# Kernel optimization log

Hardware: AMD Instinct MI355X
Metric: run time of the kernel (lower is better)

The kernel has to match this reference:

```python
import jax, jax.numpy as jnp
import numpy as np

DIM = 512
H = 4
HD = DIM // H
NPL = 2  # num_proj_layers
PS = float(np.sqrt(0.1))  # prior_strength ** 0.5


def conv1d(x, w, b):
    # x: [B,C,L], w: [O,I,3], SAME padding
    y = jax.lax.conv_general_dilated(x, w, window_strides=(1,), padding=[(1, 1)],
                                     dimension_numbers=('NCH', 'OIH', 'NCH'))
    return y + b[None, :, None]


def layernorm(x, g, b):
    m = jnp.mean(x, -1, keepdims=True)
    v = jnp.var(x, -1, keepdims=True)
    return (x - m) * jax.lax.rsqrt(v + 1e-5) * g + b


def maxpool1d(x):
    # kernel 3, stride 2, pad 1 (padded with -inf, matching torch MaxPool1d)
    return jax.lax.reduce_window(x, -jnp.inf, jax.lax.max, (1, 1, 3), (1, 1, 2),
                                 ((0, 0), (0, 0), (1, 1)))


def ds_block(x, cw, cb, g, b):
    # silu(conv) -> LN over channels -> maxpool; x: [B,C,L]
    x = jax.nn.silu(conv1d(x, cw, cb))
    x = jnp.swapaxes(layernorm(jnp.swapaxes(x, 1, 2), g, b), 1, 2)
    return maxpool1d(x)


def replicate_pad_odd(x):
    # F.pad(x, (0,0,0,1), 'replicate')[:, 1::2] on [B,S,D]
    return jnp.concatenate([x, x[:, -1:]], axis=1)[:, 1::2]


def setup_inputs() -> dict:
    key = jax.random.key(0)
    ks = jax.random.split(key, 16)
    B, Sq, Skv, C = 8, 2048, 512, DIM

    def n(k, shp, s=0.02):
        return jax.random.normal(k, shp, jnp.float32) * s

    return {
        'q_x': jax.random.normal(ks[0], (B, Sq, C), jnp.float32),
        'kv_x': jax.random.normal(ks[1], (B, Skv, C), jnp.float32),
        'q_freqs_cis': jax.random.normal(ks[2], (B, Sq, HD), jnp.float32),
        'k_freqs_cis': jax.random.normal(ks[3], (B, Skv, HD), jnp.float32),
        'mask': jnp.zeros((B, 1, (Sq + 1) // 2, Skv), jnp.float32),
        'attn_prior': jax.random.uniform(ks[4], (B, Sq, Skv), jnp.float32),
        'qds_conv_w': n(ks[5], (C, C, 3), 0.05),
        'qds_conv_b': jnp.zeros((C,), jnp.float32),
        'qds_ln_g': jnp.ones((C,), jnp.float32),
        'qds_ln_b': jnp.zeros((C,), jnp.float32),
        'qp_conv_w': n(ks[6], (NPL, C, C, 3), 0.05),
        'qp_conv_b': jnp.zeros((NPL, C), jnp.float32),
        'qp_ln_g': jnp.ones((NPL, C), jnp.float32),
        'qp_ln_b': jnp.zeros((NPL, C), jnp.float32),
        'wq': n(ks[7], (C, C)),
        'wk': n(ks[8], (C, C)),
        'wv': n(ks[9], (C, C)),
        'score_w': n(ks[10], (H, H, 45, 5), 0.02),
        'score_b': jnp.zeros((H,), jnp.float32),
        'proj_w': n(ks[11], (C, C)),
        'proj_b': jnp.zeros((C,), jnp.float32),
    }


def reference(q_x, kv_x, q_freqs_cis, k_freqs_cis, mask, attn_prior,
              qds_conv_w, qds_conv_b, qds_ln_g, qds_ln_b,
              qp_conv_w, qp_conv_b, qp_ln_g, qp_ln_b,
              wq, wk, wv, score_w, score_b, proj_w, proj_b):
    B, Sq, C = q_x.shape
    Skv = kv_x.shape[1]
    scale = HD ** -0.5

    # QueryDownsample: length Sq -> (Sq+1)//2
    x = ds_block(jnp.swapaxes(q_x, 1, 2), qds_conv_w, qds_conv_b, qds_ln_g, qds_ln_b)

    # QueryProj (note: original loop `for i in range(1, num_layers)` never uses xs[num_layers])
    xs = [x]
    for i in range(NPL):
        x = ds_block(x, qp_conv_w[i], qp_conv_b[i], qp_ln_g[i], qp_ln_b[i])
        xs.append(x)
    out = xs[0]
    for i in range(1, NPL):
        xi = jnp.repeat(xs[i], 2 ** i, axis=-1)  # nearest upsample
        out = out + xi[..., :out.shape[-1]]
    qx = jnp.swapaxes(out, 1, 2)  # [B, Sq2, C]
    Sq2 = (Sq + 1) // 2

    q = (qx @ wq.T).reshape(B, Sq2, H, HD)
    k = (kv_x @ wk.T).reshape(B, Skv, H, HD)
    v = (kv_x @ wv.T).reshape(B, Skv, H, HD)

    qf = replicate_pad_odd(q_freqs_cis)  # [B, Sq2, HD]
    q = q + qf[:, :, None] * PS
    k = k + k_freqs_cis[:, :, None] * PS

    q = jnp.swapaxes(q, 1, 2)  # [B,H,Sq2,HD]
    k = jnp.swapaxes(k, 1, 2)
    v = jnp.swapaxes(v, 1, 2)

    # gaussian attention: negative clamped squared L2 distance
    qs = q * scale
    kk = k * scale
    x2 = jnp.sum(qs * qs, -1)  # [B,H,Sq2]
    y2 = jnp.sum(kk * kk, -1)  # [B,H,Skv]
    xy = jnp.einsum('bhid,bhjd->bhij', qs, kk)
    attn = -jnp.clip(x2[..., :, None] + y2[..., None, :] - 2.0 * xy, 0.0, None)

    temp = jnp.linspace(1.0, 10.0, H).astype(attn.dtype)
    attn = attn / temp[None, :, None, None]

    # Conv2d(H,H,(45,5),padding=(22,2)) over the score map (mixes heads)
    sc = jax.lax.conv_general_dilated(attn, score_w, (1, 1), ((22, 22), (2, 2)),
                                      dimension_numbers=('NCHW', 'OIHW', 'NCHW'))
    attn = attn + sc + score_b[None, :, None, None]
    attn = attn + mask
    attn = jax.nn.softmax(attn, axis=-1)

    # prior log-fusion + renormalize
    prior = replicate_pad_odd(attn_prior)  # [B,Sq2,Skv]
    attn = jnp.exp(jnp.log(jnp.clip(attn, 1e-8, None)) +
                   jnp.log(jnp.clip(prior[:, None], 1e-8, None)))
    attn = attn / (jnp.sum(attn, -1, keepdims=True) + 1e-8)

    # nearest interpolate (Sq2 -> 2*Sq2) then crop to Sq
    attn = jnp.repeat(attn, 2, axis=2)[:, :, :Sq]  # [B,H,Sq,Skv]

    xout = jnp.einsum('bhqk,bhkd->bhqd', attn, v)
    xout = jnp.swapaxes(xout, 1, 2).reshape(B, Sq, C)
    xout = xout @ proj_w.T + proj_b
    return xout, attn
```

## Files before the change

kernel.cpp:

```cpp
#include <hip/hip_runtime.h>
#include <math.h>

#define PS_CONST 0.31622776601683794f

typedef __attribute__((ext_vector_type(8))) short short8;
typedef __attribute__((ext_vector_type(4))) float f32x4;

__device__ inline unsigned short f2b(float f) {
    unsigned u = __builtin_bit_cast(unsigned, f);
    unsigned r = (u + 0x7fffu + ((u >> 16) & 1u)) >> 16;
    return (unsigned short)r;
}
__device__ inline float b2f(unsigned short b) {
    return __builtin_bit_cast(float, (unsigned)b << 16);
}

__global__ __launch_bounds__(256) void cvt_bf16_k(const float* __restrict__ in,
                                                  ushort* __restrict__ out, int n4)
{
    int idx = blockIdx.x * 256 + threadIdx.x;
    if (idx >= n4) return;
    float4 vv = ((const float4*)in)[idx];
    ushort4 o;
    o.x = f2b(vv.x); o.y = f2b(vv.y); o.z = f2b(vv.z); o.w = f2b(vv.w);
    ((ushort4*)out)[idx] = o;
}

__global__ __launch_bounds__(256) void split_bf16_k(const float* __restrict__ in,
    ushort* __restrict__ hi, ushort* __restrict__ lo, int n4)
{
    int idx = blockIdx.x * 256 + threadIdx.x;
    if (idx >= n4) return;
    float4 vv = ((const float4*)in)[idx];
    float vs[4] = {vv.x, vv.y, vv.z, vv.w};
    ushort4 h, l;
    unsigned short hb; float hf;
    hb = f2b(vs[0]); hf = b2f(hb); h.x = hb; l.x = f2b(vs[0] - hf);
    hb = f2b(vs[1]); hf = b2f(hb); h.y = hb; l.y = f2b(vs[1] - hf);
    hb = f2b(vs[2]); hf = b2f(hb); h.z = hb; l.z = f2b(vs[2] - hf);
    hb = f2b(vs[3]); hf = b2f(hb); h.w = hb; l.w = f2b(vs[3] - hf);
    ((ushort4*)hi)[idx] = h;
    ((ushort4*)lo)[idx] = l;
}

__global__ __launch_bounds__(256) void wcvt_k(const float* __restrict__ w,
                                              ushort* __restrict__ out)
{
    int idx = blockIdx.x * 256 + threadIdx.x;
    if (idx >= 786432) return;
    int c = idx / 1536;
    int rem = idx - c * 1536;
    int tap = rem >> 9, i = rem & 511;
    out[idx] = f2b(w[c * 1536 + i * 3 + tap]);
}

__global__ __launch_bounds__(256) void wcvt4_k(
    const float* __restrict__ w0, const float* __restrict__ w1,
    const float* __restrict__ w2, const float* __restrict__ w3,
    ushort* __restrict__ o0, ushort* __restrict__ o1,
    ushort* __restrict__ o2, ushort* __restrict__ o3)
{
    int idx = blockIdx.x * 256 + threadIdx.x;
    int sel = idx >> 16, off = idx & 65535;
    const float* w = (sel == 0) ? w0 : (sel == 1) ? w1 : (sel == 2) ? w2 : w3;
    ushort* o = (sel == 0) ? o0 : (sel == 1) ? o1 : (sel == 2) ? o2 : o3;
    float4 vv = ((const float4*)w)[off];
    ushort4 r;
    r.x = f2b(vv.x); r.y = f2b(vv.y); r.z = f2b(vv.z); r.w = f2b(vv.w);
    ((ushort4*)o)[off] = r;
}

__global__ __launch_bounds__(256) void atoep_k(const float* __restrict__ sw,
                                               ushort* __restrict__ At)
{
    int idx = blockIdx.x * 256 + threadIdx.x;
    if (idx >= 81920) return;
    int t = idx & 7;
    int lane = (idx >> 3) & 63;
    int ks = (idx >> 9) & 1;
    int rem = idx >> 10;
    int dj = rem % 5, ohi = rem / 5;
    int m = lane & 15;
    int k = ks * 32 + ((lane >> 4) << 3) + t;
    int d = k - m;
    float val = (d >= 0 && d < 45) ? sw[(ohi * 45 + d) * 5 + dj] : 0.f;
    At[idx] = f2b(val);
}

__global__ __launch_bounds__(256) void conv_mfma(
    const ushort* __restrict__ xtb, const ushort* __restrict__ wtb,
    const float* __restrict__ cb, float* __restrict__ z, int L)
{
    __shared__ __align__(16) ushort Ash[128 * 40];
    __shared__ __align__(16) ushort Bsh[128 * 40];
    const int b = blockIdx.z;
    const int cm = blockIdx.y << 7;
    const int l0 = blockIdx.x << 7;
    const int tid = threadIdx.x;
    const int wave = tid >> 6, lane = tid & 63;
    const int wm = (wave & 1) << 6, wn = (wave >> 1) << 6;
    const int lo16 = lane & 15, hi4 = lane >> 4;

    f32x4 acc[4][4];
    #pragma unroll
    for (int i = 0; i < 4; i++)
        #pragma unroll
        for (int j = 0; j < 4; j++)
            acc[i][j] = (f32x4){0.f, 0.f, 0.f, 0.f};

    for (int k0 = 0; k0 < 1536; k0 += 32) {
        const int tap = k0 >> 9;
        const int cbase = k0 & 511;
        {
            int u = tid;
            #pragma unroll
            for (int p = 0; p < 2; p++, u += 256) {
                int row = u >> 2, g = (u & 3) << 3;
                *(uint4*)&Ash[row * 40 + g] =
                    *(const uint4*)&wtb[(size_t)(cm + row) * 1536 + k0 + g];
            }
        }
        {
            int u = tid;
            #pragma unroll
            for (int p = 0; p < 2; p++, u += 256) {
                int row = u >> 2, g = (u & 3) << 3;
                int lg = l0 + tap - 1 + row;
                uint4 val = make_uint4(0u, 0u, 0u, 0u);
                if (lg >= 0 && lg < L)
                    val = *(const uint4*)&xtb[((size_t)b * L + lg) * 512 + cbase + g];
                *(uint4*)&Bsh[row * 40 + g] = val;
            }
        }
        __syncthreads();
        short8 a[4], bb[4];
        #pragma unroll
        for (int t = 0; t < 4; t++) {
            a[t]  = *(const short8*)&Ash[(wm + t * 16 + lo16) * 40 + hi4 * 8];
            bb[t] = *(const short8*)&Bsh[(wn + t * 16 + lo16) * 40 + hi4 * 8];
        }
        #pragma unroll
        for (int mt = 0; mt < 4; mt++)
            #pragma unroll
            for (int nt = 0; nt < 4; nt++)
                acc[mt][nt] = __builtin_amdgcn_mfma_f32_16x16x32_bf16(
                    a[mt], bb[nt], acc[mt][nt], 0, 0, 0);
        __syncthreads();
    }
    #pragma unroll
    for (int mt = 0; mt < 4; mt++) {
        #pragma unroll
        for (int r = 0; r < 4; r++) {
            int c = cm + wm + mt * 16 + hi4 * 4 + r;
            float bias = cb[c];
            #pragma unroll
            for (int nt = 0; nt < 4; nt++) {
                int l = l0 + wn + nt * 16 + lo16;
                float u = acc[mt][nt][r] + bias;
                u = u / (1.f + __expf(-u));
                z[((size_t)b * 512 + c) * L + l] = u;
            }
        }
    }
}

__global__ __launch_bounds__(256) void gemm_mfma_bf16(
    const ushort* __restrict__ Xb, const ushort* __restrict__ Wb,
    const float* __restrict__ bias, float* __restrict__ Y,
    int M, int N, int K, int dup)
{
    __shared__ __align__(16) ushort Ash[128 * 40];
    __shared__ __align__(16) ushort Bsh[128 * 40];
    const int bm = blockIdx.y << 7, bn = blockIdx.x << 7;
    const int tid = threadIdx.x;
    const int wave = tid >> 6, lane = tid & 63;
    const int wm = (wave & 1) << 6, wn = (wave >> 1) << 6;
    const int lo16 = lane & 15, hi4 = lane >> 4;

    f32x4 acc[4][4];
    #pragma unroll
    for (int i = 0; i < 4; i++)
        #pragma unroll
        for (int j = 0; j < 4; j++)
            acc[i][j] = (f32x4){0.f, 0.f, 0.f, 0.f};

    for (int k0 = 0; k0 < K; k0 += 32) {
        int u = tid;
        #pragma unroll
        for (int p = 0; p < 2; p++, u += 256) {
            int row = u >> 2, g = (u & 3) << 3;
            *(uint4*)&Ash[row * 40 + g] =
                *(const uint4*)&Xb[(size_t)(bm + row) * K + k0 + g];
            *(uint4*)&Bsh[row * 40 + g] =
                *(const uint4*)&Wb[(size_t)(bn + row) * K + k0 + g];
        }
        __syncthreads();
        short8 a[4], bb[4];
        #pragma unroll
        for (int t = 0; t < 4; t++) {
            a[t]  = *(const short8*)&Ash[(wm + t * 16 + lo16) * 40 + hi4 * 8];
            bb[t] = *(const short8*)&Bsh[(wn + t * 16 + lo16) * 40 + hi4 * 8];
        }
        #pragma unroll
        for (int mt = 0; mt < 4; mt++)
            #pragma unroll
            for (int nt = 0; nt < 4; nt++)
                acc[mt][nt] = __builtin_amdgcn_mfma_f32_16x16x32_bf16(
                    a[mt], bb[nt], acc[mt][nt], 0, 0, 0);
        __syncthreads();
    }
    #pragma unroll
    for (int mt = 0; mt < 4; mt++) {
        #pragma unroll
        for (int r = 0; r < 4; r++) {
            int m = bm + wm + mt * 16 + hi4 * 4 + r;
            #pragma unroll
            for (int nt = 0; nt < 4; nt++) {
                int n = bn + wn + nt * 16 + lo16;
                float val = acc[mt][nt][r];
                if (bias) val += bias[n];
                if (dup) {
                    Y[(size_t)(2 * m)     * N + n] = val;
                    Y[(size_t)(2 * m + 1) * N + n] = val;
                } else {
                    Y[(size_t)m * N + n] = val;
                }
            }
        }
    }
}

__global__ __launch_bounds__(256) void ln_stats_k(const float* __restrict__ z,
                                                  float2* __restrict__ stats, int L)
{
    __shared__ float s_sh[4][64];
    __shared__ float s2_sh[4][64];
    const int b = blockIdx.y;
    const int colL = threadIdx.x & 63;
    const int col = (blockIdx.x << 6) + colL;
    const int part = threadIdx.x >> 6;
    const float* base = z + ((size_t)b * 512 + part * 128) * L + col;
    float s = 0.f, s2 = 0.f;
    for (int i = 0; i < 128; i++) {
        float vv = base[(size_t)i * L];
        s += vv; s2 += vv * vv;
    }
    s_sh[part][colL] = s; s2_sh[part][colL] = s2;
    __syncthreads();
    if (threadIdx.x < 64) {
        float ts = 0.f, ts2 = 0.f;
        #pragma unroll
        for (int p = 0; p < 4; p++) { ts += s_sh[p][colL]; ts2 += s2_sh[p][colL]; }
        float m = ts * (1.f / 512.f);
        float var = ts2 * (1.f / 512.f) - m * m;
        stats[(size_t)b * L + col] = make_float2(m, rsqrtf(var + 1e-5f));
    }
}

__global__ __launch_bounds__(256) void ln_maxpool_k(
    const float* __restrict__ z, const float2* __restrict__ stats,
    const float* __restrict__ g, const float* __restrict__ be,
    float* __restrict__ out, int L, int lshift)
{
    const int Lout = 1 << lshift;
    size_t idx = (size_t)blockIdx.x * 256 + threadIdx.x;
    int lp = (int)(idx & (Lout - 1));
    int c = (int)((idx >> lshift) & 511);
    int b = (int)(idx >> (lshift + 9));
    const float* zp = z + ((size_t)b * 512 + c) * L;
    const float2* sp = stats + (size_t)b * L;
    float gc = g[c], bc = be[c];
    int l = lp << 1;
    float2 st = sp[l];
    float m = (zp[l] - st.x) * st.y * gc + bc;
    if (l > 0) {
        float2 s0 = sp[l - 1];
        m = fmaxf(m, (zp[l - 1] - s0.x) * s0.y * gc + bc);
    }
    float2 s1 = sp[l + 1];
    m = fmaxf(m, (zp[l + 1] - s1.x) * s1.y * gc + bc);
    out[idx] = m;
}

__global__ __launch_bounds__(256) void transpose_cvt_k(const float* __restrict__ x0,
                                                       ushort* __restrict__ xtb)
{
    __shared__ ushort t[32][33];
    const int b = blockIdx.z, c0 = blockIdx.y << 5, l0 = blockIdx.x << 5;
    const int col = threadIdx.x & 31, r0 = threadIdx.x >> 5;
    #pragma unroll
    for (int p = 0; p < 4; p++) {
        int r = r0 + p * 8;
        t[r][col] = f2b(x0[((size_t)b * 512 + c0 + r) * 1024 + l0 + col]);
    }
    __syncthreads();
    #pragma unroll
    for (int p = 0; p < 4; p++) {
        int r = r0 + p * 8;
        xtb[((size_t)b * 1024 + l0 + r) * 512 + c0 + col] = t[col][r];
    }
}

__global__ __launch_bounds__(256) void vT_cvt_k(const float* __restrict__ v,
                                                ushort* __restrict__ vTb)
{
    __shared__ ushort t[32][33];
    const int bh = blockIdx.z, b = bh >> 2, h = bh & 3;
    const int d0 = blockIdx.y << 5, j0 = blockIdx.x << 5;
    const int col = threadIdx.x & 31, r0 = threadIdx.x >> 5;
    #pragma unroll
    for (int p = 0; p < 4; p++) {
        int r = r0 + p * 8;
        t[r][col] = f2b(v[(((size_t)b * 512 + j0 + r) * 4 + h) * 128 + d0 + col]);
    }
    __syncthreads();
    #pragma unroll
    for (int p = 0; p < 4; p++) {
        int r = r0 + p * 8;
        vTb[((size_t)bh * 128 + d0 + r) * 512 + j0 + col] = t[col][r];
    }
}

__global__ __launch_bounds__(256) void upsample_add_t(const float* __restrict__ x0,
    const float* __restrict__ x1, ushort* __restrict__ qxb)
{
    size_t idx = (size_t)blockIdx.x * 256 + threadIdx.x;
    int c = (int)(idx & 511);
    int l = (int)((idx >> 9) & 1023);
    int b = (int)(idx >> 19);
    qxb[idx] = f2b(x0[((size_t)b * 512 + c) * 1024 + l] +
                   x1[((size_t)b * 512 + c) * 512 + (l >> 1)]);
}

__global__ __launch_bounds__(256) void add_freq_q_k(float* __restrict__ q, const float* __restrict__ qf)
{
    size_t idx = (size_t)blockIdx.x * 256 + threadIdx.x;
    int d = (int)(idx & 127);
    int l = (int)((idx >> 9) & 1023);
    int b = (int)(idx >> 19);
    q[idx] += PS_CONST * qf[((size_t)b * 2048 + 2 * l + 1) * 128 + d];
}

__global__ __launch_bounds__(256) void add_freq_k_k(float* __restrict__ k, const float* __restrict__ kf)
{
    size_t idx = (size_t)blockIdx.x * 256 + threadIdx.x;
    int d = (int)(idx & 127);
    int j = (int)((idx >> 9) & 511);
    int b = (int)(idx >> 18);
    k[idx] += PS_CONST * kf[((size_t)b * 512 + j) * 128 + d];
}

__global__ __launch_bounds__(64) void rownorm_k(const float* __restrict__ X,
                                                float* __restrict__ out, int Li)
{
    int i = blockIdx.x, bh = blockIdx.y;
    int b = bh >> 2, h = bh & 3;
    const float* row = X + (((size_t)b * Li + i) * 4 + h) * 128;
    int lane = threadIdx.x;
    float v0 = row[lane], v1 = row[lane + 64];
    float s = v0 * v0 + v1 * v1;
    #pragma unroll
    for (int off = 32; off > 0; off >>= 1) s += __shfl_down(s, off);
    if (lane == 0) out[(size_t)bh * Li + i] = s;
}

__global__ __launch_bounds__(256) void scores_mfma(
    const ushort* __restrict__ qhi, const ushort* __restrict__ qlo,
    const ushort* __restrict__ khi, const ushort* __restrict__ klo,
    const float* __restrict__ q2, const float* __restrict__ k2,
    float* __restrict__ attn0)
{
    __shared__ __align__(16) ushort Ah[128 * 40];
    __shared__ __align__(16) ushort Al[128 * 40];
    __shared__ __align__(16) ushort Bh[128 * 40];
    __shared__ __align__(16) ushort Bl[128 * 40];
    const int bh = blockIdx.z, b = bh >> 2, h = bh & 3;
    const int bm = blockIdx.y << 7, bn = blockIdx.x << 7;
    const int tid = threadIdx.x;
    const int wave = tid >> 6, lane = tid & 63;
    const int wm = (wave & 1) << 6, wn = (wave >> 1) << 6;
    const int lo16 = lane & 15, hi4 = lane >> 4;

    f32x4 acc[4][4];
    #pragma unroll
    for (int i = 0; i < 4; i++)
        #pragma unroll
        for (int j = 0; j < 4; j++)
            acc[i][j] = (f32x4){0.f, 0.f, 0.f, 0.f};

    for (int k0 = 0; k0 < 128; k0 += 32) {
        int u = tid;
        #pragma unroll
        for (int p = 0; p < 2; p++, u += 256) {
            int row = u >> 2, g = (u & 3) << 3;
            size_t aoff = (((size_t)b * 1024 + bm + row) * 4 + h) * 128 + k0 + g;
            size_t boff = (((size_t)b * 512  + bn + row) * 4 + h) * 128 + k0 + g;
            *(uint4*)&Ah[row * 40 + g] = *(const uint4*)&qhi[aoff];
            *(uint4*)&Al[row * 40 + g] = *(const uint4*)&qlo[aoff];
            *(uint4*)&Bh[row * 40 + g] = *(const uint4*)&khi[boff];
            *(uint4*)&Bl[row * 40 + g] = *(const uint4*)&klo[boff];
        }
        __syncthreads();
        short8 ah[4], al[4], bhF[4], blF[4];
        #pragma unroll
        for (int t = 0; t < 4; t++) {
            int ar = (wm + t * 16 + lo16) * 40 + hi4 * 8;
            int br = (wn + t * 16 + lo16) * 40 + hi4 * 8;
            ah[t]  = *(const short8*)&Ah[ar];
            al[t]  = *(const short8*)&Al[ar];
            bhF[t] = *(const short8*)&Bh[br];
            blF[t] = *(const short8*)&Bl[br];
        }
        #pragma unroll
        for (int mt = 0; mt < 4; mt++)
            #pragma unroll
            for (int nt = 0; nt < 4; nt++) {
                acc[mt][nt] = __builtin_amdgcn_mfma_f32_16x16x32_bf16(
                    ah[mt], bhF[nt], acc[mt][nt], 0, 0, 0);
                acc[mt][nt] = __builtin_amdgcn_mfma_f32_16x16x32_bf16(
                    ah[mt], blF[nt], acc[mt][nt], 0, 0, 0);
                acc[mt][nt] = __builtin_amdgcn_mfma_f32_16x16x32_bf16(
                    al[mt], bhF[nt], acc[mt][nt], 0, 0, 0);
            }
        __syncthreads();
    }
    const float it = (h == 0) ? 1.f : (h == 1) ? 0.25f : (h == 2) ? (1.f / 7.f) : 0.1f;
    #pragma unroll
    for (int mt = 0; mt < 4; mt++) {
        #pragma unroll
        for (int r = 0; r < 4; r++) {
            int i = bm + wm + mt * 16 + hi4 * 4 + r;
            float q2v = q2[(size_t)bh * 1024 + i];
            #pragma unroll
            for (int nt = 0; nt < 4; nt++) {
                int j = bn + wn + nt * 16 + lo16;
                float d2 = q2v + k2[(size_t)bh * 512 + j] - 2.f * acc[mt][nt][r];
                d2 *= (1.f / 128.f);
                if (d2 < 0.f) d2 = 0.f;
                attn0[((size_t)bh * 1024 + i) * 512 + j] = -d2 * it;
            }
        }
    }
}

__global__ __launch_bounds__(256) void score_conv_mfma(
    const float* __restrict__ attn0, const ushort* __restrict__ At,
    const float* __restrict__ sb, const float* __restrict__ mask,
    float* __restrict__ attn1)
{
    __shared__ __align__(16) ushort tileT[4 * 36 * 120];
    const int b = blockIdx.z, i0 = blockIdx.y << 6, j0 = blockIdx.x << 5;
    const int tid = threadIdx.x, wave = tid >> 6, lane = tid & 63;

    for (int idx = tid; idx < 4 * 36 * 56; idx += 256) {
        int jj = idx % 36;
        int r2 = idx / 36;
        int ip = r2 % 56, hi = r2 / 56;
        int ii = ip << 1;
        int gi = i0 - 22 + ii, gj = j0 - 2 + jj;
        const float* src = attn0 + ((size_t)(b * 4 + hi) * 1024 + gi) * 512 + gj;
        bool jv = (unsigned)gj < 512u;
        float v0 = (jv && (unsigned)gi       < 1024u) ? src[0]   : 0.f;
        float v1 = (jv && (unsigned)(gi + 1) < 1024u) ? src[512] : 0.f;
        unsigned pk = (unsigned)f2b(v0) | ((unsigned)f2b(v1) << 16);
        *(unsigned*)&tileT[(hi * 36 + jj) * 120 + ii] = pk;
    }
    __syncthreads();

    const int n16 = lane & 15, quad = lane >> 4;
    f32x4 acc[4][2];
    #pragma unroll
    for (int o = 0; o < 4; o++)
        #pragma unroll
        for (int t = 0; t < 2; t++)
            acc[o][t] = (f32x4){0.f, 0.f, 0.f, 0.f};

    const int iibase = wave * 16 + quad * 8;
    #pragma unroll 1
    for (int hi = 0; hi < 4; hi++) {
        #pragma unroll 1
        for (int dj = 0; dj < 5; dj++) {
            #pragma unroll
            for (int ks = 0; ks < 2; ks++) {
                short8 bf[2];
                #pragma unroll
                for (int t = 0; t < 2; t++)
                    bf[t] = *(const short8*)&tileT[(hi * 36 + t * 16 + n16 + dj) * 120
                                                   + iibase + ks * 32];
                #pragma unroll
                for (int o = 0; o < 4; o++) {
                    short8 af = *(const short8*)&At[((((o * 4 + hi) * 5 + dj) * 2 + ks) * 64
                                                     + lane) * 8];
                    #pragma unroll
                    for (int t = 0; t < 2; t++)
                        acc[o][t] = __builtin_amdgcn_mfma_f32_16x16x32_bf16(
                            af, bf[t], acc[o][t], 0, 0, 0);
                }
            }
        }
    }

    #pragma unroll
    for (int o = 0; o < 4; o++) {
        float bo = sb[o];
        #pragma unroll
        for (int r = 0; r < 4; r++) {
            int i = i0 + wave * 16 + quad * 4 + r;
            size_t obase = ((size_t)(b * 4 + o) * 1024 + i) * 512;
            size_t mbase = ((size_t)b * 1024 + i) * 512;
            #pragma unroll
            for (int t = 0; t < 2; t++) {
                int j = j0 + t * 16 + n16;
                attn1[obase + j] = attn0[obase + j] + acc[o][t][r] + bo + mask[mbase + j];
            }
        }
    }
}

__global__ __launch_bounds__(256) void softmax_prior_k(
    const float* __restrict__ attn1, const float* __restrict__ prior,
    float* __restrict__ attn_out, ushort* __restrict__ ab)
{
    const int wid = threadIdx.x >> 6, lane = threadIdx.x & 63;
    size_t row = (size_t)blockIdx.x * 4 + wid;
    int i = (int)(row & 1023);
    int bh = (int)(row >> 10);
    int b = bh >> 2;
    const float* arow = attn1 + row * 512;
    const float* prow = prior + ((size_t)b * 2048 + 2 * i + 1) * 512;
    float v[8], p[8];
    #pragma unroll
    for (int t = 0; t < 8; t++) {
        v[t] = arow[lane + 64 * t];
        p[t] = prow[lane + 64 * t];
    }
    float mx = v[0];
    #pragma unroll
    for (int t = 1; t < 8; t++) mx = fmaxf(mx, v[t]);
    #pragma unroll
    for (int off = 32; off > 0; off >>= 1) mx = fmaxf(mx, __shfl_xor(mx, off));
    float sum = 0.f;
    #pragma unroll
    for (int t = 0; t < 8; t++) { v[t] = expf(v[t] - mx); sum += v[t]; }
    #pragma unroll
    for (int off = 32; off > 0; off >>= 1) sum += __shfl_xor(sum, off);
    float inv = 1.f / sum;
    float sum2 = 0.f;
    #pragma unroll
    for (int t = 0; t < 8; t++) {
        float sm = fmaxf(v[t] * inv, 1e-8f);
        float pr = fmaxf(p[t], 1e-8f);
        v[t] = sm * pr;
        sum2 += v[t];
    }
    #pragma unroll
    for (int off = 32; off > 0; off >>= 1) sum2 += __shfl_xor(sum2, off);
    float inv2 = 1.f / (sum2 + 1e-8f);
    float* o0 = attn_out + ((size_t)bh * 2048 + 2 * i) * 512;
    ushort* abrow = ab + row * 512;
    #pragma unroll
    for (int t = 0; t < 8; t++) {
        float val = v[t] * inv2;
        o0[lane + 64 * t] = val;
        o0[512 + lane + 64 * t] = val;
        abrow[lane + 64 * t] = f2b(val);
    }
}

__global__ __launch_bounds__(256) void attnv_mfma(
    const ushort* __restrict__ ab, const ushort* __restrict__ vTb,
    ushort* __restrict__ xpb)
{
    __shared__ __align__(16) ushort Ash[128 * 40];
    __shared__ __align__(16) ushort Bsh[128 * 40];
    const int bh = blockIdx.z, b = bh >> 2, h = bh & 3;
    const int bm = blockIdx.y << 7;
    const ushort* A = ab + (size_t)bh * 1024 * 512;
    const ushort* B = vTb + (size_t)bh * 128 * 512;
    const int tid = threadIdx.x;
    const int wave = tid >> 6, lane = tid & 63;
    const int wm = (wave & 1) << 6, wn = (wave >> 1) << 6;
    const int lo16 = lane & 15, hi4 = lane >> 4;

    f32x4 acc[4][4];
    #pragma unroll
    for (int i = 0; i < 4; i++)
        #pragma unroll
        for (int j = 0; j < 4; j++)
            acc[i][j] = (f32x4){0.f, 0.f, 0.f, 0.f};

    for (int k0 = 0; k0 < 512; k0 += 32) {
        int u = tid;
        #pragma unroll
        for (int p = 0; p < 2; p++, u += 256) {
            int row = u >> 2, g = (u & 3) << 3;
            *(uint4*)&Ash[row * 40 + g] = *(const uint4*)&A[(size_t)(bm + row) * 512 + k0 + g];
            *(uint4*)&Bsh[row * 40 + g] = *(const uint4*)&B[(size_t)row * 512 + k0 + g];
        }
        __syncthreads();
        short8 a[4], bb[4];
        #pragma unroll
        for (int t = 0; t < 4; t++) {
            a[t]  = *(const short8*)&Ash[(wm + t * 16 + lo16) * 40 + hi4 * 8];
            bb[t] = *(const short8*)&Bsh[(wn + t * 16 + lo16) * 40 + hi4 * 8];
        }
        #pragma unroll
        for (int mt = 0; mt < 4; mt++)
            #pragma unroll
            for (int nt = 0; nt < 4; nt++)
                acc[mt][nt] = __builtin_amdgcn_mfma_f32_16x16x32_bf16(
                    a[mt], bb[nt], acc[mt][nt], 0, 0, 0);
        __syncthreads();
    }
    #pragma unroll
    for (int mt = 0; mt < 4; mt++) {
        #pragma unroll
        for (int r = 0; r < 4; r++) {
            int m = bm + wm + mt * 16 + hi4 * 4 + r;
            #pragma unroll
            for (int nt = 0; nt < 4; nt++) {
                int n = wn + nt * 16 + lo16;
                xpb[((size_t)b * 1024 + m) * 512 + h * 128 + n] = f2b(acc[mt][nt][r]);
            }
        }
    }
}

extern "C" void kernel_launch(void* const* d_in, const int* in_sizes, int n_in,
                              void* d_out, int out_size, void* d_ws, size_t ws_size,
                              hipStream_t stream)
{
    const float* q_x    = (const float*)d_in[0];
    const float* kv_x   = (const float*)d_in[1];
    const float* qf     = (const float*)d_in[2];
    const float* kf     = (const float*)d_in[3];
    const float* mask   = (const float*)d_in[4];
    const float* prior  = (const float*)d_in[5];
    const float* qds_w  = (const float*)d_in[6];
    const float* qds_b  = (const float*)d_in[7];
    const float* qds_g  = (const float*)d_in[8];
    const float* qds_be = (const float*)d_in[9];
    const float* qp_w   = (const float*)d_in[10];
    const float* qp_b   = (const float*)d_in[11];
    const float* qp_g   = (const float*)d_in[12];
    const float* qp_be  = (const float*)d_in[13];
    const float* wq     = (const float*)d_in[14];
    const float* wk     = (const float*)d_in[15];
    const float* wv     = (const float*)d_in[16];
    const float* sw     = (const float*)d_in[17];
    const float* sb     = (const float*)d_in[18];
    const float* pw     = (const float*)d_in[19];
    const float* pb     = (const float*)d_in[20];

    if (ws_size < (size_t)56672256 * 4) return;
    float* ws = (float*)d_ws;
    float* z     = ws;
    float* x0    = ws + 8388608;
    float* x1    = ws + 12582912;
    float* q     = ws + 14680064;
    float* k     = ws + 18874368;
    float* v     = ws + 20971520;
    float* q2    = ws + 23068672;
    float* k2    = ws + 23101440;
    float* attn0 = ws + 23117824;
    float* attn1 = ws + 39895040;
    ushort* xtb   = (ushort*)(ws + 39895040);
    ushort* x0tb  = (ushort*)(ws + 39895040 + 4194304);
    ushort* wc1b  = (ushort*)(ws + 39895040 + 6291456);
    ushort* wc2b  = (ushort*)(ws + 39895040 + 6684672);
    float2* stats1 = (float2*)(ws + 39895040 + 7077888);
    float2* stats2 = (float2*)(ws + 39895040 + 7110656);
    ushort* qxb  = (ushort*)z;
    ushort* At   = (ushort*)x0;
    ushort* wqb  = (ushort*)(ws + 8454144);
    ushort* wkb  = (ushort*)(ws + 8585216);
    ushort* wvb  = (ushort*)(ws + 8716288);
    ushort* pwb  = (ushort*)(ws + 8847360);
    ushort* khi  = (ushort*)(ws + 8978432);
    ushort* klo  = (ushort*)(ws + 10027008);
    ushort* vTb  = (ushort*)(ws + 11075584);
    ushort* kvb  = (ushort*)x1;
    ushort* qhi  = (ushort*)z;
    ushort* qlo  = (ushort*)(ws + 2097152);
    ushort* xpb  = (ushort*)attn0;
    ushort* ab   = (ushort*)(ws + 25214976);

    float* out_x    = (float*)d_out;
    float* out_attn = out_x + (size_t)8 * 2048 * 512;

    cvt_bf16_k<<<8192, 256, 0, stream>>>(q_x, xtb, 2097152);
    wcvt_k<<<3072, 256, 0, stream>>>(qds_w, wc1b);
    wcvt_k<<<3072, 256, 0, stream>>>(qp_w, wc2b);
    conv_mfma<<<dim3(16, 4, 8), 256, 0, stream>>>(xtb, wc1b, qds_b, z, 2048);
    ln_stats_k<<<dim3(32, 8), 256, 0, stream>>>(z, stats1, 2048);
    ln_maxpool_k<<<16384, 256, 0, stream>>>(z, stats1, qds_g, qds_be, x0, 2048, 10);
    transpose_cvt_k<<<dim3(32, 16, 8), 256, 0, stream>>>(x0, x0tb);
    conv_mfma<<<dim3(8, 4, 8), 256, 0, stream>>>(x0tb, wc2b, qp_b, z, 1024);
    ln_stats_k<<<dim3(16, 8), 256, 0, stream>>>(z, stats2, 1024);
    ln_maxpool_k<<<8192, 256, 0, stream>>>(z, stats2, qp_g, qp_be, x1, 1024, 9);
    upsample_add_t<<<16384, 256, 0, stream>>>(x0, x1, qxb);
    atoep_k<<<320, 256, 0, stream>>>(sw, At);
    wcvt4_k<<<1024, 256, 0, stream>>>(wq, wk, wv, pw, wqb, wkb, wvb, pwb);
    cvt_bf16_k<<<2048, 256, 0, stream>>>(kv_x, kvb, 524288);
    gemm_mfma_bf16<<<dim3(4, 64), 256, 0, stream>>>(qxb, wqb, nullptr, q, 8192, 512, 512, 0);
    gemm_mfma_bf16<<<dim3(4, 32), 256, 0, stream>>>(kvb, wkb, nullptr, k, 4096, 512, 512, 0);
    gemm_mfma_bf16<<<dim3(4, 32), 256, 0, stream>>>(kvb, wvb, nullptr, v, 4096, 512, 512, 0);
    add_freq_q_k<<<16384, 256, 0, stream>>>(q, qf);
    add_freq_k_k<<<8192, 256, 0, stream>>>(k, kf);
    rownorm_k<<<dim3(1024, 32), 64, 0, stream>>>(q, q2, 1024);
    rownorm_k<<<dim3(512, 32), 64, 0, stream>>>(k, k2, 512);
    split_bf16_k<<<4096, 256, 0, stream>>>(q, qhi, qlo, 1048576);
    split_bf16_k<<<2048, 256, 0, stream>>>(k, khi, klo, 524288);
    vT_cvt_k<<<dim3(16, 4, 32), 256, 0, stream>>>(v, vTb);
    scores_mfma<<<dim3(4, 8, 32), 256, 0, stream>>>(qhi, qlo, khi, klo, q2, k2, attn0);
    score_conv_mfma<<<dim3(16, 16, 8), 256, 0, stream>>>(attn0, At, sb, mask, attn1);
    softmax_prior_k<<<8192, 256, 0, stream>>>(attn1, prior, out_attn, ab);
    attnv_mfma<<<dim3(1, 8, 32), 256, 0, stream>>>(ab, vTb, xpb);
    gemm_mfma_bf16<<<dim3(4, 64), 256, 0, stream>>>(xpb, pwb, pb, out_x, 8192, 512, 512, 1);
}
```

Baseline: 762.4 us.

## Fuse freq add into projection GEMMs, merge rownorm with split, shrink score-conv tile

Adds the scaled frequency tensors in the Q/K projection GEMM epilogue, which removes two elementwise read-modify-write passes over q and k. The row-norm reduction is merged into the hi/lo bf16 split kernel, so q and k are read once instead of twice. The score-conv kernel tile width drops from 32 to 16 columns, doubling the grid. This gives more blocks and less LDS per block, but the halo overhead per output grows and each A-fragment load now feeds only one MFMA.

```diff
diff --git a/kernel.cpp b/kernel.cpp
--- a/kernel.cpp
+++ b/kernel.cpp
@@ -26,21 +26,31 @@
     ((ushort4*)out)[idx] = o;
 }
 
-__global__ __launch_bounds__(256) void split_bf16_k(const float* __restrict__ in,
-    ushort* __restrict__ hi, ushort* __restrict__ lo, int n4)
-{
-    int idx = blockIdx.x * 256 + threadIdx.x;
-    if (idx >= n4) return;
-    float4 vv = ((const float4*)in)[idx];
-    float vs[4] = {vv.x, vv.y, vv.z, vv.w};
-    ushort4 h, l;
-    unsigned short hb; float hf;
-    hb = f2b(vs[0]); hf = b2f(hb); h.x = hb; l.x = f2b(vs[0] - hf);
-    hb = f2b(vs[1]); hf = b2f(hb); h.y = hb; l.y = f2b(vs[1] - hf);
-    hb = f2b(vs[2]); hf = b2f(hb); h.z = hb; l.z = f2b(vs[2] - hf);
-    hb = f2b(vs[3]); hf = b2f(hb); h.w = hb; l.w = f2b(vs[3] - hf);
-    ((ushort4*)hi)[idx] = h;
-    ((ushort4*)lo)[idx] = l;
+__global__ __launch_bounds__(256) void split_norm_k(const float* __restrict__ X,
+    ushort* __restrict__ hi, ushort* __restrict__ lo, float* __restrict__ out2,
+    int lishift)
+{
+    int row = blockIdx.x * 4 + (threadIdx.x >> 6);
+    int lane = threadIdx.x & 63;
+    const float* rp = X + (size_t)row * 128;
+    float v0 = rp[lane], v1 = rp[lane + 64];
+    unsigned short h0 = f2b(v0); float hf0 = b2f(h0);
+    unsigned short l0 = f2b(v0 - hf0);
+    unsigned short h1 = f2b(v1); float hf1 = b2f(h1);
+    unsigned short l1 = f2b(v1 - hf1);
+    hi[(size_t)row * 128 + lane]      = h0;
+    hi[(size_t)row * 128 + lane + 64] = h1;
+    lo[(size_t)row * 128 + lane]      = l0;
+    lo[(size_t)row * 128 + lane + 64] = l1;
+    float s = v0 * v0 + v1 * v1;
+    #pragma unroll
+    for (int off = 32; off > 0; off >>= 1) s += __shfl_down(s, off);
+    if (lane == 0) {
+        int h = row & 3;
+        int i = (row >> 2) & ((1 << lishift) - 1);
+        int b = row >> (lishift + 2);
+        out2[(((size_t)b * 4 + h) << lishift) + i] = s;
+    }
 }
 
 __global__ __launch_bounds__(256) void wcvt_k(const float* __restrict__ w,
@@ -167,7 +177,8 @@
 __global__ __launch_bounds__(256) void gemm_mfma_bf16(
     const ushort* __restrict__ Xb, const ushort* __restrict__ Wb,
     const float* __restrict__ bias, float* __restrict__ Y,
-    int M, int N, int K, int dup)
+    int M, int N, int K, int dup,
+    const float* __restrict__ freq, int mshift, int fF, int dupfreq)
 {
     __shared__ __align__(16) ushort Ash[128 * 40];
     __shared__ __align__(16) ushort Bsh[128 * 40];
@@ -214,11 +225,19 @@
         #pragma unroll
         for (int r = 0; r < 4; r++) {
             int m = bm + wm + mt * 16 + hi4 * 4 + r;
+            const float* frow = nullptr;
+            if (freq) {
+                int fb = m >> mshift;
+                int fl = m & ((1 << mshift) - 1);
+                int fr = dupfreq ? (2 * fl + 1) : fl;
+                frow = freq + ((size_t)fb * fF + fr) * 128;
+            }
             #pragma unroll
             for (int nt = 0; nt < 4; nt++) {
                 int n = bn + wn + nt * 16 + lo16;
                 float val = acc[mt][nt][r];
                 if (bias) val += bias[n];
+                if (freq) val += PS_CONST * frow[n & 127];
                 if (dup) {
                     Y[(size_t)(2 * m)     * N + n] = val;
                     Y[(size_t)(2 * m + 1) * N + n] = val;
@@ -332,38 +351,6 @@
                    x1[((size_t)b * 512 + c) * 512 + (l >> 1)]);
 }
 
-__global__ __launch_bounds__(256) void add_freq_q_k(float* __restrict__ q, const float* __restrict__ qf)
-{
-    size_t idx = (size_t)blockIdx.x * 256 + threadIdx.x;
-    int d = (int)(idx & 127);
-    int l = (int)((idx >> 9) & 1023);
-    int b = (int)(idx >> 19);
-    q[idx] += PS_CONST * qf[((size_t)b * 2048 + 2 * l + 1) * 128 + d];
-}
-
-__global__ __launch_bounds__(256) void add_freq_k_k(float* __restrict__ k, const float* __restrict__ kf)
-{
-    size_t idx = (size_t)blockIdx.x * 256 + threadIdx.x;
-    int d = (int)(idx & 127);
-    int j = (int)((idx >> 9) & 511);
-    int b = (int)(idx >> 18);
-    k[idx] += PS_CONST * kf[((size_t)b * 512 + j) * 128 + d];
-}
-
-__global__ __launch_bounds__(64) void rownorm_k(const float* __restrict__ X,
-                                                float* __restrict__ out, int Li)
-{
-    int i = blockIdx.x, bh = blockIdx.y;
-    int b = bh >> 2, h = bh & 3;
-    const float* row = X + (((size_t)b * Li + i) * 4 + h) * 128;
-    int lane = threadIdx.x;
-    float v0 = row[lane], v1 = row[lane + 64];
-    float s = v0 * v0 + v1 * v1;
-    #pragma unroll
-    for (int off = 32; off > 0; off >>= 1) s += __shfl_down(s, off);
-    if (lane == 0) out[(size_t)bh * Li + i] = s;
-}
-
 __global__ __launch_bounds__(256) void scores_mfma(
     const ushort* __restrict__ qhi, const ushort* __restrict__ qlo,
     const ushort* __restrict__ khi, const ushort* __restrict__ klo,
@@ -448,13 +435,13 @@
     const float* __restrict__ sb, const float* __restrict__ mask,
     float* __restrict__ attn1)
 {
-    __shared__ __align__(16) ushort tileT[4 * 36 * 120];
-    const int b = blockIdx.z, i0 = blockIdx.y << 6, j0 = blockIdx.x << 5;
+    __shared__ __align__(16) ushort tileT[4 * 20 * 120];
+    const int b = blockIdx.z, i0 = blockIdx.y << 6, j0 = blockIdx.x << 4;
     const int tid = threadIdx.x, wave = tid >> 6, lane = tid & 63;
 
-    for (int idx = tid; idx < 4 * 36 * 56; idx += 256) {
-        int jj = idx % 36;
-        int r2 = idx / 36;
+    for (int idx = tid; idx < 4 * 20 * 56; idx += 256) {
+        int jj = idx % 20;
+        int r2 = idx / 20;
         int ip = r2 % 56, hi = r2 / 56;
         int ii = ip << 1;
         int gi = i0 - 22 + ii, gj = j0 - 2 + jj;
@@ -463,17 +450,15 @@
         float v0 = (jv && (unsigned)gi       < 1024u) ? src[0]   : 0.f;
         float v1 = (jv && (unsigned)(gi + 1) < 1024u) ? src[512] : 0.f;
         unsigned pk = (unsigned)f2b(v0) | ((unsigned)f2b(v1) << 16);
-        *(unsigned*)&tileT[(hi * 36 + jj) * 120 + ii] = pk;
+        *(unsigned*)&tileT[(hi * 20 + jj) * 120 + ii] = pk;
     }
     __syncthreads();
 
     const int n16 = lane & 15, quad = lane >> 4;
-    f32x4 acc[4][2];
+    f32x4 acc[4];
     #pragma unroll
     for (int o = 0; o < 4; o++)
-        #pragma unroll
-        for (int t = 0; t < 2; t++)
-            acc[o][t] = (f32x4){0.f, 0.f, 0.f, 0.f};
+        acc[o] = (f32x4){0.f, 0.f, 0.f, 0.f};
 
     const int iibase = wave * 16 + quad * 8;
     #pragma unroll 1
@@ -482,19 +467,14 @@
         for (int dj = 0; dj < 5; dj++) {
             #pragma unroll
             for (int ks = 0; ks < 2; ks++) {
-                short8 bf[2];
-                #pragma unroll
-                for (int t = 0; t < 2; t++)
-                    bf[t] = *(const short8*)&tileT[(hi * 36 + t * 16 + n16 + dj) * 120
+                short8 bf = *(const short8*)&tileT[(hi * 20 + n16 + dj) * 120
                                                    + iibase + ks * 32];
                 #pragma unroll
                 for (int o = 0; o < 4; o++) {
                     short8 af = *(const short8*)&At[((((o * 4 + hi) * 5 + dj) * 2 + ks) * 64
                                                      + lane) * 8];
-                    #pragma unroll
-                    for (int t = 0; t < 2; t++)
-                        acc[o][t] = __builtin_amdgcn_mfma_f32_16x16x32_bf16(
-                            af, bf[t], acc[o][t], 0, 0, 0);
+                    acc[o] = __builtin_amdgcn_mfma_f32_16x16x32_bf16(
+                        af, bf, acc[o], 0, 0, 0);
                 }
             }
         }
@@ -508,11 +488,8 @@
             int i = i0 + wave * 16 + quad * 4 + r;
             size_t obase = ((size_t)(b * 4 + o) * 1024 + i) * 512;
             size_t mbase = ((size_t)b * 1024 + i) * 512;
-            #pragma unroll
-            for (int t = 0; t < 2; t++) {
-                int j = j0 + t * 16 + n16;
-                attn1[obase + j] = attn0[obase + j] + acc[o][t][r] + bo + mask[mbase + j];
-            }
+            int j = j0 + n16;
+            attn1[obase + j] = attn0[obase + j] + acc[o][r] + bo + mask[mbase + j];
         }
     }
 }
@@ -702,19 +679,19 @@
     atoep_k<<<320, 256, 0, stream>>>(sw, At);
     wcvt4_k<<<1024, 256, 0, stream>>>(wq, wk, wv, pw, wqb, wkb, wvb, pwb);
     cvt_bf16_k<<<2048, 256, 0, stream>>>(kv_x, kvb, 524288);
-    gemm_mfma_bf16<<<dim3(4, 64), 256, 0, stream>>>(qxb, wqb, nullptr, q, 8192, 512, 512, 0);
-    gemm_mfma_bf16<<<dim3(4, 32), 256, 0, stream>>>(kvb, wkb, nullptr, k, 4096, 512, 512, 0);
-    gemm_mfma_bf16<<<dim3(4, 32), 256, 0, stream>>>(kvb, wvb, nullptr, v, 4096, 512, 512, 0);
-    add_freq_q_k<<<16384, 256, 0, stream>>>(q, qf);
-    add_freq_k_k<<<8192, 256, 0, stream>>>(k, kf);
-    rownorm_k<<<dim3(1024, 32), 64, 0, stream>>>(q, q2, 1024);
-    rownorm_k<<<dim3(512, 32), 64, 0, stream>>>(k, k2, 512);
-    split_bf16_k<<<4096, 256, 0, stream>>>(q, qhi, qlo, 1048576);
-    split_bf16_k<<<2048, 256, 0, stream>>>(k, khi, klo, 524288);
+    gemm_mfma_bf16<<<dim3(4, 64), 256, 0, stream>>>(qxb, wqb, nullptr, q, 8192, 512, 512, 0,
+                                                    qf, 10, 2048, 1);
+    gemm_mfma_bf16<<<dim3(4, 32), 256, 0, stream>>>(kvb, wkb, nullptr, k, 4096, 512, 512, 0,
+                                                    kf, 9, 512, 0);
+    gemm_mfma_bf16<<<dim3(4, 32), 256, 0, stream>>>(kvb, wvb, nullptr, v, 4096, 512, 512, 0,
+                                                    nullptr, 0, 0, 0);
+    split_norm_k<<<8192, 256, 0, stream>>>(q, qhi, qlo, q2, 10);
+    split_norm_k<<<4096, 256, 0, stream>>>(k, khi, klo, k2, 9);
     vT_cvt_k<<<dim3(16, 4, 32), 256, 0, stream>>>(v, vTb);
     scores_mfma<<<dim3(4, 8, 32), 256, 0, stream>>>(qhi, qlo, khi, klo, q2, k2, attn0);
-    score_conv_mfma<<<dim3(16, 16, 8), 256, 0, stream>>>(attn0, At, sb, mask, attn1);
+    score_conv_mfma<<<dim3(32, 16, 8), 256, 0, stream>>>(attn0, At, sb, mask, attn1);
     softmax_prior_k<<<8192, 256, 0, stream>>>(attn1, prior, out_attn, ab);
     attnv_mfma<<<dim3(1, 8, 32), 256, 0, stream>>>(ab, vTb, xpb);
-    gemm_mfma_bf16<<<dim3(4, 64), 256, 0, stream>>>(xpb, pwb, pb, out_x, 8192, 512, 512, 1);
-}
+    gemm_mfma_bf16<<<dim3(4, 64), 256, 0, stream>>>(xpb, pwb, pb, out_x, 8192, 512, 512, 1,
+                                                    nullptr, 0, 0, 0);
+}
```

Measured after the change: 817.0 us. 7.2% more time.
